# Kernel tuning notes

Hardware: AMD Instinct MI355X
Metric: run time of the kernel (lower is better)

Reference implementation:

```python
import jax, jax.numpy as jnp
import numpy as np

IN_CAPS, IN_SIZE = 1152, 8
OUT_CAPS, OUT_SIZE = 10, 16
NUM_ITERS = 3


def squash(s, axis=-1, eps=1e-8):
    sq = jnp.sum(s * s, axis=axis, keepdims=True)
    norm = jnp.sqrt(sq + eps)
    return (sq / (1.0 + sq)) * (s / norm)


def setup_inputs() -> dict:
    key = jax.random.key(0)
    kx, kw = jax.random.split(key)
    x = jax.random.normal(kx, (512, IN_CAPS, IN_SIZE), dtype=jnp.float32)
    W = jax.random.normal(kw, (IN_CAPS, OUT_CAPS, OUT_SIZE, IN_SIZE), dtype=jnp.float32)
    return {"x": x, "W": W}


def reference(x, W):
    # u_hat[b,i,o,p] = sum_q W[i,o,p,q] x[b,i,q]   -> [B, I, O, P]
    u_hat = jnp.einsum("iopq,biq->biop", W, x)
    b_ij = jnp.zeros((IN_CAPS, OUT_CAPS), dtype=u_hat.dtype)
    v_j = None
    for _ in range(NUM_ITERS):
        # legacy F.softmax on [1,I,O,1] with no dim -> softmax over dim=1 (in_capsules)
        c_ij = jax.nn.softmax(b_ij, axis=0)                      # [I, O]
        s_j = jnp.einsum("io,biop->bop", c_ij, u_hat)            # [B, O, P]
        v_j = squash(s_j, axis=-1)                               # [B, O, P]
        # agreement, averaged over batch
        u_vj1 = jnp.einsum("biop,bop->io", u_hat, v_j) / x.shape[0]
        b_ij = b_ij + u_vj1
    return v_j  # [B, 10, 16]
```

## Files before the change

### kernel.cpp

```cpp
#include <hip/hip_runtime.h>
#include <hip/hip_bf16.h>

#define B 512
#define IC 1152
#define QD 8
#define OD 10
#define PD 16
#define KD (IC * QD)
#define NKB (KD / 32)
#define NCS 24
#define KSTEPS (NKB / NCS)
#define NCB 16
#define CSB (B / NCB)
#define SOP (B * OD * PD)

typedef short bf16x8 __attribute__((ext_vector_type(8)));
typedef float f32x4 __attribute__((ext_vector_type(4)));

__device__ __forceinline__ short f2bf(float f) {
  union { float f; unsigned u; } x;
  x.f = f;
  unsigned r = x.u + 0x7FFFu + ((x.u >> 16) & 1u);
  return (short)(r >> 16);
}

__global__ __launch_bounds__(256) void init_c_kernel(float* __restrict__ c) {
  const int t = blockIdx.x * 256 + threadIdx.x;
  if (t < IC * OD) c[t] = 1.0f / (float)IC;
}

__global__ __launch_bounds__(256) void build_b_kernel(const float* __restrict__ W,
                                                      const float* __restrict__ c,
                                                      short* __restrict__ Bs) {
  const int t = blockIdx.x * 256 + threadIdx.x;
  if (t >= NKB * 160) return;
  const int kb = t / 160, n = t % 160;
  const int o = n >> 4, p = n & 15;
  short ov[32];
#pragma unroll
  for (int quad = 0; quad < 4; ++quad) {
    const int i = kb * 4 + quad;
    const float ci = c[i * OD + o];
    const float4* wp = (const float4*)(W + (((size_t)i * OD + o) * PD + p) * QD);
    const float4 w0 = wp[0], w1 = wp[1];
    ov[quad * 8 + 0] = f2bf(ci * w0.x);
    ov[quad * 8 + 1] = f2bf(ci * w0.y);
    ov[quad * 8 + 2] = f2bf(ci * w0.z);
    ov[quad * 8 + 3] = f2bf(ci * w0.w);
    ov[quad * 8 + 4] = f2bf(ci * w1.x);
    ov[quad * 8 + 5] = f2bf(ci * w1.y);
    ov[quad * 8 + 6] = f2bf(ci * w1.z);
    ov[quad * 8 + 7] = f2bf(ci * w1.w);
  }
  int4* dst = (int4*)(Bs + (size_t)t * 32);
  const int4* src = (const int4*)ov;
#pragma unroll
  for (int j = 0; j < 4; ++j) dst[j] = src[j];
}

__global__ __launch_bounds__(256) void sgemm_kernel(const float* __restrict__ x,
                                                    const short* __restrict__ Bs,
                                                    float* __restrict__ s_part) {
  const int lane = threadIdx.x & 63;
  const int w = threadIdx.x >> 6;
  const int ln = lane & 15, quad = lane >> 4;
  const int m0 = blockIdx.x * 64 + w * 16;
  const int nb = blockIdx.y * 80;
  const int cz = blockIdx.z;
  f32x4 acc[5] = {};
  const float* arow = x + (size_t)(m0 + ln) * KD + quad * 8;
#pragma unroll 2
  for (int step = 0; step < KSTEPS; ++step) {
    const int kb = cz * KSTEPS + step;
    const float* ap = arow + kb * 32;
    const f32x4 a0 = *(const f32x4*)ap;
    const f32x4 a1 = *(const f32x4*)(ap + 4);
    bf16x8 af;
    af[0] = f2bf(a0[0]); af[1] = f2bf(a0[1]); af[2] = f2bf(a0[2]); af[3] = f2bf(a0[3]);
    af[4] = f2bf(a1[0]); af[5] = f2bf(a1[1]); af[6] = f2bf(a1[2]); af[7] = f2bf(a1[3]);
    const short* bp = Bs + (size_t)kb * 5120 + (nb + ln) * 32 + quad * 8;
#pragma unroll
    for (int nt = 0; nt < 5; ++nt) {
      const bf16x8 bf = *(const bf16x8*)(bp + nt * 512);
      acc[nt] = __builtin_amdgcn_mfma_f32_16x16x32_bf16(af, bf, acc[nt], 0, 0, 0);
    }
  }
  float* sp = s_part + (size_t)cz * SOP;
#pragma unroll
  for (int nt = 0; nt < 5; ++nt) {
#pragma unroll
    for (int r = 0; r < 4; ++r) {
      sp[(size_t)(m0 + quad * 4 + r) * 160 + nb + nt * 16 + ln] = acc[nt][r];
    }
  }
}

__global__ __launch_bounds__(256) void squash_kernel(const float* __restrict__ s_part,
                                                     float* __restrict__ v,
                                                     float* __restrict__ out,
                                                     int write_out) {
  const int t = blockIdx.x * 256 + threadIdx.x;
  float sv = 0.f;
#pragma unroll
  for (int ch = 0; ch < NCS; ++ch) sv += s_part[(size_t)ch * SOP + t];
  float sq = sv * sv;
#pragma unroll
  for (int m = 1; m < 16; m <<= 1) sq += __shfl_xor(sq, m, 16);
  const float norm = sqrtf(sq + 1e-8f);
  const float val = sv * (sq / ((1.f + sq) * norm));
  v[t] = val;
  if (write_out) out[t] = val;
}

__global__ __launch_bounds__(320) void agree_kernel(const float* __restrict__ x,
                                                    const float* __restrict__ W,
                                                    const float* __restrict__ v,
                                                    float* __restrict__ u_part) {
  const int il = threadIdx.x >> 3;
  const int q = threadIdx.x & 7;
  const int i = blockIdx.x * 8 + il;
  const int b0 = blockIdx.y * CSB;
  const int o1 = threadIdx.y;
  const int o2 = threadIdx.y + 5;
  float G0[PD], G1[PD];
#pragma unroll
  for (int p = 0; p < PD; ++p) { G0[p] = 0.f; G1[p] = 0.f; }
  for (int b = b0; b < b0 + CSB; ++b) {
    const float xa = x[((size_t)b * IC + i) * QD + q];
    const int vo0 = __builtin_amdgcn_readfirstlane((b * OD + o1) * PD);
    const int vo1 = __builtin_amdgcn_readfirstlane((b * OD + o2) * PD);
    const float4* vp0 = (const float4*)(v + vo0);
    const float4* vp1 = (const float4*)(v + vo1);
    const float4 a0 = vp0[0], a1 = vp0[1], a2 = vp0[2], a3 = vp0[3];
    const float4 c0 = vp1[0], c1 = vp1[1], c2 = vp1[2], c3 = vp1[3];
    const float va[PD] = {a0.x, a0.y, a0.z, a0.w, a1.x, a1.y, a1.z, a1.w,
                          a2.x, a2.y, a2.z, a2.w, a3.x, a3.y, a3.z, a3.w};
    const float vc[PD] = {c0.x, c0.y, c0.z, c0.w, c1.x, c1.y, c1.z, c1.w,
                          c2.x, c2.y, c2.z, c2.w, c3.x, c3.y, c3.z, c3.w};
#pragma unroll
    for (int p = 0; p < PD; ++p) G0[p] = fmaf(xa, va[p], G0[p]);
#pragma unroll
    for (int p = 0; p < PD; ++p) G1[p] = fmaf(xa, vc[p], G1[p]);
  }
  const float* wq1 = W + ((size_t)(i * OD + o1) * PD) * QD + q;
  const float* wq2 = W + ((size_t)(i * OD + o2) * PD) * QD + q;
  float u0 = 0.f, u1 = 0.f;
#pragma unroll
  for (int p = 0; p < PD; ++p) {
    u0 = fmaf(wq1[(size_t)p * QD], G0[p], u0);
    u1 = fmaf(wq2[(size_t)p * QD], G1[p], u1);
  }
  u0 += __shfl_xor(u0, 1); u0 += __shfl_xor(u0, 2); u0 += __shfl_xor(u0, 4);
  u1 += __shfl_xor(u1, 1); u1 += __shfl_xor(u1, 2); u1 += __shfl_xor(u1, 4);
  if (q == 0) {
    float* up = u_part + ((size_t)blockIdx.y * IC + i) * OD;
    up[o1] = u0 * (1.0f / (float)B);
    up[o2] = u1 * (1.0f / (float)B);
  }
}

__global__ __launch_bounds__(256) void route_kernel(const float* __restrict__ u_part,
                                                    float* __restrict__ bij,
                                                    float* __restrict__ c,
                                                    int add_prev) {
  const int o = blockIdx.x;
  __shared__ float red[256];
  float val[5];
  float lmax = -1e30f;
#pragma unroll
  for (int k = 0; k < 5; ++k) {
    const int i = threadIdx.x + k * 256;
    if (i < IC) {
      float sacc = add_prev ? bij[i * OD + o] : 0.f;
#pragma unroll
      for (int ch = 0; ch < NCB; ++ch) sacc += u_part[((size_t)ch * IC + i) * OD + o];
      val[k] = sacc;
      bij[i * OD + o] = sacc;
      lmax = fmaxf(lmax, sacc);
    } else {
      val[k] = -1e30f;
    }
  }
  red[threadIdx.x] = lmax;
  __syncthreads();
  for (int st = 128; st > 0; st >>= 1) {
    if (threadIdx.x < st) red[threadIdx.x] = fmaxf(red[threadIdx.x], red[threadIdx.x + st]);
    __syncthreads();
  }
  const float gmax = red[0];
  __syncthreads();
  float lsum = 0.f;
#pragma unroll
  for (int k = 0; k < 5; ++k) {
    const int i = threadIdx.x + k * 256;
    if (i < IC) {
      val[k] = __expf(val[k] - gmax);
      lsum += val[k];
    }
  }
  red[threadIdx.x] = lsum;
  __syncthreads();
  for (int st = 128; st > 0; st >>= 1) {
    if (threadIdx.x < st) red[threadIdx.x] += red[threadIdx.x + st];
    __syncthreads();
  }
  const float inv = 1.f / red[0];
#pragma unroll
  for (int k = 0; k < 5; ++k) {
    const int i = threadIdx.x + k * 256;
    if (i < IC) c[i * OD + o] = val[k] * inv;
  }
}

extern "C" void kernel_launch(void* const* d_in, const int* in_sizes, int n_in,
                              void* d_out, int out_size, void* d_ws, size_t ws_size,
                              hipStream_t stream) {
  const float* x = (const float*)d_in[0];
  const float* W = (const float*)d_in[1];
  float* out = (float*)d_out;

  float* ws = (float*)d_ws;
  float* s_part = ws;
  float* v = s_part + (size_t)NCS * SOP;
  float* bij = v + SOP;
  float* c = bij + IC * OD;
  short* Bs = (short*)(c + IC * OD);
  float* u_part = (float*)Bs;

  const dim3 ggrid(8, 2, NCS), gblk(256);
  const dim3 agrid(IC / 8, NCB), ablk(64, 5);

  init_c_kernel<<<(IC * OD + 255) / 256, 256, 0, stream>>>(c);
  for (int iter = 0; iter < 3; ++iter) {
    build_b_kernel<<<(NKB * 160 + 255) / 256, 256, 0, stream>>>(W, c, Bs);
    sgemm_kernel<<<ggrid, gblk, 0, stream>>>(x, Bs, s_part);
    squash_kernel<<<SOP / 256, 256, 0, stream>>>(s_part, v, out, iter == 2);
    if (iter < 2) {
      agree_kernel<<<agrid, ablk, 0, stream>>>(x, W, v, u_part);
      route_kernel<<<OD, 256, 0, stream>>>(u_part, bij, c, iter > 0);
    }
  }
}
```

Baseline: 209.5 us.

## Fuse softmax routing into B-build, rebalance sgemm split-K and agree tiling

Merges the route (softmax over input capsules) and build_b kernels into one routebuild kernel. Every block redundantly recomputes the full softmax in shared memory, so the separate c buffer, init kernel and route launch go away. The sgemm now covers all 160 output columns per block and raises the split-K factor from 24 to 72 chunks, trading more partial-sum traffic in squash for more parallel blocks. The agree kernel stages x tiles in LDS and loops over output pairs per wave, which cuts redundant x loads; the redundant softmax work per block is the added cost.

```diff
diff --git a/kernel.cpp b/kernel.cpp
--- a/kernel.cpp
+++ b/kernel.cpp
@@ -8,11 +8,12 @@
 #define PD 16
 #define KD (IC * QD)
 #define NKB (KD / 32)
-#define NCS 24
+#define NCS 72
 #define KSTEPS (NKB / NCS)
 #define NCB 16
 #define CSB (B / NCB)
 #define SOP (B * OD * PD)
+#define IO (IC * OD)
 
 typedef short bf16x8 __attribute__((ext_vector_type(8)));
 typedef float f32x4 __attribute__((ext_vector_type(4)));
@@ -24,33 +25,99 @@
   return (short)(r >> 16);
 }
 
-__global__ __launch_bounds__(256) void init_c_kernel(float* __restrict__ c) {
-  const int t = blockIdx.x * 256 + threadIdx.x;
-  if (t < IC * OD) c[t] = 1.0f / (float)IC;
-}
-
-__global__ __launch_bounds__(256) void build_b_kernel(const float* __restrict__ W,
-                                                      const float* __restrict__ c,
-                                                      short* __restrict__ Bs) {
-  const int t = blockIdx.x * 256 + threadIdx.x;
-  if (t >= NKB * 160) return;
+__global__ __launch_bounds__(256) void routebuild_kernel(const float* __restrict__ W,
+                                                         const float* __restrict__ u_part,
+                                                         float* __restrict__ bijA,
+                                                         short* __restrict__ Bs,
+                                                         int mode) {
+  __shared__ float bl[IO];
+  __shared__ float wred[4][OD];
+  __shared__ float mx[OD], inv[OD];
+  const int tid = threadIdx.x;
+  const int wave = tid >> 6, lane = tid & 63;
+
+  if (mode != 0) {
+    float lmax[OD];
+#pragma unroll
+    for (int o = 0; o < OD; ++o) lmax[o] = -1e30f;
+    for (int i = tid; i < IC; i += 256) {
+      float acc[OD];
+      if (mode == 2) {
+#pragma unroll
+        for (int o = 0; o < OD; ++o) acc[o] = bijA[i * OD + o];
+      } else {
+#pragma unroll
+        for (int o = 0; o < OD; ++o) acc[o] = 0.f;
+      }
+      for (int bc = 0; bc < NCB; ++bc) {
+        const float* up = u_part + (size_t)bc * IO + i * OD;
+        const float4 u0 = *(const float4*)up;
+        const float4 u1 = *(const float4*)(up + 4);
+        const float2 u2 = *(const float2*)(up + 8);
+        acc[0] += u0.x; acc[1] += u0.y; acc[2] += u0.z; acc[3] += u0.w;
+        acc[4] += u1.x; acc[5] += u1.y; acc[6] += u1.z; acc[7] += u1.w;
+        acc[8] += u2.x; acc[9] += u2.y;
+      }
+#pragma unroll
+      for (int o = 0; o < OD; ++o) {
+        bl[i * OD + o] = acc[o];
+        lmax[o] = fmaxf(lmax[o], acc[o]);
+        if (mode == 1 && blockIdx.x == 0) bijA[i * OD + o] = acc[o];
+      }
+    }
+#pragma unroll
+    for (int o = 0; o < OD; ++o) {
+      float m = lmax[o];
+#pragma unroll
+      for (int s = 1; s < 64; s <<= 1) m = fmaxf(m, __shfl_xor(m, s));
+      if (lane == 0) wred[wave][o] = m;
+    }
+    __syncthreads();
+    if (tid < OD) {
+      mx[tid] = fmaxf(fmaxf(wred[0][tid], wred[1][tid]),
+                      fmaxf(wred[2][tid], wred[3][tid]));
+    }
+    __syncthreads();
+    float lsum[OD];
+#pragma unroll
+    for (int o = 0; o < OD; ++o) lsum[o] = 0.f;
+    for (int i = tid; i < IC; i += 256) {
+#pragma unroll
+      for (int o = 0; o < OD; ++o) {
+        const float e = __expf(bl[i * OD + o] - mx[o]);
+        bl[i * OD + o] = e;
+        lsum[o] += e;
+      }
+    }
+    __syncthreads();
+#pragma unroll
+    for (int o = 0; o < OD; ++o) {
+      float s = lsum[o];
+#pragma unroll
+      for (int st = 1; st < 64; st <<= 1) s += __shfl_xor(s, st);
+      if (lane == 0) wred[wave][o] = s;
+    }
+    __syncthreads();
+    if (tid < OD) {
+      inv[tid] = 1.f / (wred[0][tid] + wred[1][tid] + wred[2][tid] + wred[3][tid]);
+    }
+    __syncthreads();
+  }
+
+  const int t = blockIdx.x * 256 + tid;
   const int kb = t / 160, n = t % 160;
   const int o = n >> 4, p = n & 15;
   short ov[32];
 #pragma unroll
   for (int quad = 0; quad < 4; ++quad) {
     const int i = kb * 4 + quad;
-    const float ci = c[i * OD + o];
+    const float ci = (mode == 0) ? (1.0f / (float)IC) : (bl[i * OD + o] * inv[o]);
     const float4* wp = (const float4*)(W + (((size_t)i * OD + o) * PD + p) * QD);
     const float4 w0 = wp[0], w1 = wp[1];
-    ov[quad * 8 + 0] = f2bf(ci * w0.x);
-    ov[quad * 8 + 1] = f2bf(ci * w0.y);
-    ov[quad * 8 + 2] = f2bf(ci * w0.z);
-    ov[quad * 8 + 3] = f2bf(ci * w0.w);
-    ov[quad * 8 + 4] = f2bf(ci * w1.x);
-    ov[quad * 8 + 5] = f2bf(ci * w1.y);
-    ov[quad * 8 + 6] = f2bf(ci * w1.z);
-    ov[quad * 8 + 7] = f2bf(ci * w1.w);
+    ov[quad * 8 + 0] = f2bf(ci * w0.x); ov[quad * 8 + 1] = f2bf(ci * w0.y);
+    ov[quad * 8 + 2] = f2bf(ci * w0.z); ov[quad * 8 + 3] = f2bf(ci * w0.w);
+    ov[quad * 8 + 4] = f2bf(ci * w1.x); ov[quad * 8 + 5] = f2bf(ci * w1.y);
+    ov[quad * 8 + 6] = f2bf(ci * w1.z); ov[quad * 8 + 7] = f2bf(ci * w1.w);
   }
   int4* dst = (int4*)(Bs + (size_t)t * 32);
   const int4* src = (const int4*)ov;
@@ -61,15 +128,14 @@
 __global__ __launch_bounds__(256) void sgemm_kernel(const float* __restrict__ x,
                                                     const short* __restrict__ Bs,
                                                     float* __restrict__ s_part) {
-  const int lane = threadIdx.x & 63;
-  const int w = threadIdx.x >> 6;
+  const int tid = threadIdx.x;
+  const int wave = tid >> 6, lane = tid & 63;
   const int ln = lane & 15, quad = lane >> 4;
-  const int m0 = blockIdx.x * 64 + w * 16;
-  const int nb = blockIdx.y * 80;
-  const int cz = blockIdx.z;
-  f32x4 acc[5] = {};
+  const int cz = blockIdx.x % NCS, mb = blockIdx.x / NCS;
+  const int m0 = mb * 64 + wave * 16;
+  f32x4 acc[10] = {};
   const float* arow = x + (size_t)(m0 + ln) * KD + quad * 8;
-#pragma unroll 2
+#pragma unroll
   for (int step = 0; step < KSTEPS; ++step) {
     const int kb = cz * KSTEPS + step;
     const float* ap = arow + kb * 32;
@@ -78,21 +144,19 @@
     bf16x8 af;
     af[0] = f2bf(a0[0]); af[1] = f2bf(a0[1]); af[2] = f2bf(a0[2]); af[3] = f2bf(a0[3]);
     af[4] = f2bf(a1[0]); af[5] = f2bf(a1[1]); af[6] = f2bf(a1[2]); af[7] = f2bf(a1[3]);
-    const short* bp = Bs + (size_t)kb * 5120 + (nb + ln) * 32 + quad * 8;
-#pragma unroll
-    for (int nt = 0; nt < 5; ++nt) {
+    const short* bp = Bs + (size_t)kb * 5120 + ln * 32 + quad * 8;
+#pragma unroll
+    for (int nt = 0; nt < 10; ++nt) {
       const bf16x8 bf = *(const bf16x8*)(bp + nt * 512);
       acc[nt] = __builtin_amdgcn_mfma_f32_16x16x32_bf16(af, bf, acc[nt], 0, 0, 0);
     }
   }
   float* sp = s_part + (size_t)cz * SOP;
 #pragma unroll
-  for (int nt = 0; nt < 5; ++nt) {
-#pragma unroll
-    for (int r = 0; r < 4; ++r) {
-      sp[(size_t)(m0 + quad * 4 + r) * 160 + nb + nt * 16 + ln] = acc[nt][r];
-    }
-  }
+  for (int nt = 0; nt < 10; ++nt)
+#pragma unroll
+    for (int r = 0; r < 4; ++r)
+      sp[(size_t)(m0 + quad * 4 + r) * 160 + nt * 16 + ln] = acc[nt][r];
 }
 
 __global__ __launch_bounds__(256) void squash_kernel(const float* __restrict__ s_part,
@@ -101,7 +165,7 @@
                                                      int write_out) {
   const int t = blockIdx.x * 256 + threadIdx.x;
   float sv = 0.f;
-#pragma unroll
+#pragma unroll 8
   for (int ch = 0; ch < NCS; ++ch) sv += s_part[(size_t)ch * SOP + t];
   float sq = sv * sv;
 #pragma unroll
@@ -112,105 +176,67 @@
   if (write_out) out[t] = val;
 }
 
-__global__ __launch_bounds__(320) void agree_kernel(const float* __restrict__ x,
+__global__ __launch_bounds__(256) void agree_kernel(const float* __restrict__ x,
                                                     const float* __restrict__ W,
                                                     const float* __restrict__ v,
                                                     float* __restrict__ u_part) {
-  const int il = threadIdx.x >> 3;
-  const int q = threadIdx.x & 7;
-  const int i = blockIdx.x * 8 + il;
-  const int b0 = blockIdx.y * CSB;
-  const int o1 = threadIdx.y;
-  const int o2 = threadIdx.y + 5;
-  float G0[PD], G1[PD];
-#pragma unroll
-  for (int p = 0; p < PD; ++p) { G0[p] = 0.f; G1[p] = 0.f; }
-  for (int b = b0; b < b0 + CSB; ++b) {
-    const float xa = x[((size_t)b * IC + i) * QD + q];
-    const int vo0 = __builtin_amdgcn_readfirstlane((b * OD + o1) * PD);
-    const int vo1 = __builtin_amdgcn_readfirstlane((b * OD + o2) * PD);
-    const float4* vp0 = (const float4*)(v + vo0);
-    const float4* vp1 = (const float4*)(v + vo1);
-    const float4 a0 = vp0[0], a1 = vp0[1], a2 = vp0[2], a3 = vp0[3];
-    const float4 c0 = vp1[0], c1 = vp1[1], c2 = vp1[2], c3 = vp1[3];
-    const float va[PD] = {a0.x, a0.y, a0.z, a0.w, a1.x, a1.y, a1.z, a1.w,
-                          a2.x, a2.y, a2.z, a2.w, a3.x, a3.y, a3.z, a3.w};
-    const float vc[PD] = {c0.x, c0.y, c0.z, c0.w, c1.x, c1.y, c1.z, c1.w,
-                          c2.x, c2.y, c2.z, c2.w, c3.x, c3.y, c3.z, c3.w};
-#pragma unroll
-    for (int p = 0; p < PD; ++p) G0[p] = fmaf(xa, va[p], G0[p]);
-#pragma unroll
-    for (int p = 0; p < PD; ++p) G1[p] = fmaf(xa, vc[p], G1[p]);
-  }
-  const float* wq1 = W + ((size_t)(i * OD + o1) * PD) * QD + q;
-  const float* wq2 = W + ((size_t)(i * OD + o2) * PD) * QD + q;
-  float u0 = 0.f, u1 = 0.f;
-#pragma unroll
-  for (int p = 0; p < PD; ++p) {
-    u0 = fmaf(wq1[(size_t)p * QD], G0[p], u0);
-    u1 = fmaf(wq2[(size_t)p * QD], G1[p], u1);
-  }
-  u0 += __shfl_xor(u0, 1); u0 += __shfl_xor(u0, 2); u0 += __shfl_xor(u0, 4);
-  u1 += __shfl_xor(u1, 1); u1 += __shfl_xor(u1, 2); u1 += __shfl_xor(u1, 4);
-  if (q == 0) {
-    float* up = u_part + ((size_t)blockIdx.y * IC + i) * OD;
-    up[o1] = u0 * (1.0f / (float)B);
-    up[o2] = u1 * (1.0f / (float)B);
-  }
-}
-
-__global__ __launch_bounds__(256) void route_kernel(const float* __restrict__ u_part,
-                                                    float* __restrict__ bij,
-                                                    float* __restrict__ c,
-                                                    int add_prev) {
-  const int o = blockIdx.x;
-  __shared__ float red[256];
-  float val[5];
-  float lmax = -1e30f;
-#pragma unroll
-  for (int k = 0; k < 5; ++k) {
-    const int i = threadIdx.x + k * 256;
-    if (i < IC) {
-      float sacc = add_prev ? bij[i * OD + o] : 0.f;
-#pragma unroll
-      for (int ch = 0; ch < NCB; ++ch) sacc += u_part[((size_t)ch * IC + i) * OD + o];
-      val[k] = sacc;
-      bij[i * OD + o] = sacc;
-      lmax = fmaxf(lmax, sacc);
-    } else {
-      val[k] = -1e30f;
-    }
-  }
-  red[threadIdx.x] = lmax;
+  __shared__ __align__(16) float xs[128 * 64];
+  const int tid = threadIdx.x;
+  const int wave = tid >> 6, lane = tid & 63;
+  const int il = lane >> 3, q = lane & 7;
+  const int ig = blockIdx.x >> 2, bquad = blockIdx.x & 3;
+  const int bbase = bquad * 128;
+  const int i = ig * 8 + il;
+  for (int idx = tid; idx < 2048; idx += 256) {
+    const int row = idx >> 4, f4 = idx & 15;
+    *(float4*)(xs + row * 64 + f4 * 4) =
+        *(const float4*)(x + (size_t)(bbase + row) * KD + ig * 64 + f4 * 4);
+  }
   __syncthreads();
-  for (int st = 128; st > 0; st >>= 1) {
-    if (threadIdx.x < st) red[threadIdx.x] = fmaxf(red[threadIdx.x], red[threadIdx.x + st]);
-    __syncthreads();
-  }
-  const float gmax = red[0];
-  __syncthreads();
-  float lsum = 0.f;
-#pragma unroll
-  for (int k = 0; k < 5; ++k) {
-    const int i = threadIdx.x + k * 256;
-    if (i < IC) {
-      val[k] = __expf(val[k] - gmax);
-      lsum += val[k];
-    }
-  }
-  red[threadIdx.x] = lsum;
-  __syncthreads();
-  for (int st = 128; st > 0; st >>= 1) {
-    if (threadIdx.x < st) red[threadIdx.x] += red[threadIdx.x + st];
-    __syncthreads();
-  }
-  const float inv = 1.f / red[0];
-#pragma unroll
-  for (int k = 0; k < 5; ++k) {
-    const int i = threadIdx.x + k * 256;
-    if (i < IC) c[i * OD + o] = val[k] * inv;
-  }
-}
+  const int bc = bquad * 4 + wave;
+  const int b0 = bc * CSB;
+  const float* xw = xs + wave * 32 * 64 + il * 8 + q;
+#pragma unroll
+  for (int opair = 0; opair < 5; ++opair) {
+    const int o1 = opair, o2 = opair + 5;
+    float G0[PD], G1[PD];
+#pragma unroll
+    for (int p = 0; p < PD; ++p) { G0[p] = 0.f; G1[p] = 0.f; }
+    for (int b = 0; b < CSB; ++b) {
+      const float xa = xw[b * 64];
+      const int vo0 = __builtin_amdgcn_readfirstlane(((b0 + b) * OD + o1) * PD);
+      const int vo1 = __builtin_amdgcn_readfirstlane(((b0 + b) * OD + o2) * PD);
+      const float4* vp0 = (const float4*)(v + vo0);
+      const float4* vp1 = (const float4*)(v + vo1);
+      const float4 a0 = vp0[0], a1 = vp0[1], a2 = vp0[2], a3 = vp0[3];
+      const float4 c0 = vp1[0], c1 = vp1[1], c2 = vp1[2], c3 = vp1[3];
+      const float va[PD] = {a0.x, a0.y, a0.z, a0.w, a1.x, a1.y, a1.z, a1.w,
+                            a2.x, a2.y, a2.z, a2.w, a3.x, a3.y, a3.z, a3.w};
+      const float vc[PD] = {c0.x, c0.y, c0.z, c0.w, c1.x, c1.y, c1.z, c1.w,
+                            c2.x, c2.y, c2.z, c2.w, c3.x, c3.y, c3.z, c3.w};
+#pragma unroll
+      for (int p = 0; p < PD; ++p) G0[p] = fmaf(xa, va[p], G0[p]);
+#pragma unroll
+      for (int p = 0; p < PD; ++p) G1[p] = fmaf(xa, vc[p], G1[p]);
+    }
+    const float* wq1 = W + ((size_t)(i * OD + o1) * PD) * QD + q;
+    const float* wq2 = W + ((size_t)(i * OD + o2) * PD) * QD + q;
+    float u0s = 0.f, u1s = 0.f;
+#pragma unroll
+    for (int p = 0; p < PD; ++p) {
+      u0s = fmaf(wq1[(size_t)p * QD], G0[p], u0s);
+      u1s = fmaf(wq2[(size_t)p * QD], G1[p], u1s);
+    }
+    u0s += __shfl_xor(u0s, 1); u0s += __shfl_xor(u0s, 2); u0s += __shfl_xor(u0s, 4);
+    u1s += __shfl_xor(u1s, 1); u1s += __shfl_xor(u1s, 2); u1s += __shfl_xor(u1s, 4);
+    if (q == 0) {
+      float* up = u_part + ((size_t)bc * IC + i) * OD;
+      up[o1] = u0s * (1.0f / (float)B);
+      up[o2] = u1s * (1.0f / (float)B);
+    }
+  }
+}
+
 
 extern "C" void kernel_launch(void* const* d_in, const int* in_sizes, int n_in,
                               void* d_out, int out_size, void* d_ws, size_t ws_size,
@@ -222,22 +248,19 @@
   float* ws = (float*)d_ws;
   float* s_part = ws;
   float* v = s_part + (size_t)NCS * SOP;
-  float* bij = v + SOP;
-  float* c = bij + IC * OD;
-  short* Bs = (short*)(c + IC * OD);
-  float* u_part = (float*)Bs;
-
-  const dim3 ggrid(8, 2, NCS), gblk(256);
-  const dim3 agrid(IC / 8, NCB), ablk(64, 5);
-
-  init_c_kernel<<<(IC * OD + 255) / 256, 256, 0, stream>>>(c);
-  for (int iter = 0; iter < 3; ++iter) {
-    build_b_kernel<<<(NKB * 160 + 255) / 256, 256, 0, stream>>>(W, c, Bs);
-    sgemm_kernel<<<ggrid, gblk, 0, stream>>>(x, Bs, s_part);
-    squash_kernel<<<SOP / 256, 256, 0, stream>>>(s_part, v, out, iter == 2);
-    if (iter < 2) {
-      agree_kernel<<<agrid, ablk, 0, stream>>>(x, W, v, u_part);
-      route_kernel<<<OD, 256, 0, stream>>>(u_part, bij, c, iter > 0);
-    }
-  }
-}
+  float* bijA = v + SOP;
+  float* u_part = bijA + IO;
+  short* Bs = (short*)(u_part + (size_t)NCB * IO);
+
+  routebuild_kernel<<<180, 256, 0, stream>>>(W, u_part, bijA, Bs, 0);
+  sgemm_kernel<<<8 * NCS, 256, 0, stream>>>(x, Bs, s_part);
+  squash_kernel<<<SOP / 256, 256, 0, stream>>>(s_part, v, out, 0);
+  agree_kernel<<<576, 256, 0, stream>>>(x, W, v, u_part);
+  routebuild_kernel<<<180, 256, 0, stream>>>(W, u_part, bijA, Bs, 1);
+  sgemm_kernel<<<8 * NCS, 256, 0, stream>>>(x, Bs, s_part);
+  squash_kernel<<<SOP / 256, 256, 0, stream>>>(s_part, v, out, 0);
+  agree_kernel<<<576, 256, 0, stream>>>(x, W, v, u_part);
+  routebuild_kernel<<<180, 256, 0, stream>>>(W, u_part, bijA, Bs, 2);
+  sgemm_kernel<<<8 * NCS, 256, 0, stream>>>(x, Bs, s_part);
+  squash_kernel<<<SOP / 256, 256, 0, stream>>>(s_part, v, out, 1);
+}
```

Result: slower. 248.9 us (+18.8%).
